# Kernel optimization log

Hardware: AMD Instinct MI355X
Metric: run time of the kernel (lower is better)

Reference implementation:

```python
import jax, jax.numpy as jnp
import numpy as np

N, B, NPG, DEG, F = 16384, 128, 128, 8, 128
E = N * DEG
H1, C1, H2, C2, H3, C3 = 3, 128, 2, 64, 2, 32
D = H1 * C1 + H2 * C2 + C3  # 544
K = 30
ND = 2048
LAMDA = 0.8


def _gatv2(x, src, dst, Wl, Wr, att, b, h, c, concat):
    n = x.shape[0]
    xl = (x @ Wl).reshape(n, h, c)
    xr = (x @ Wr).reshape(n, h, c)
    e = jax.nn.leaky_relu(xl[src] + xr[dst], 0.2)           # [E+N, h, c]
    logit = jnp.einsum('ehc,hc->eh', e, att)
    m = jax.lax.stop_gradient(jax.ops.segment_max(logit, dst, num_segments=n))
    a = jnp.exp(logit - m[dst])
    z = jax.ops.segment_sum(a, dst, num_segments=n)
    a = a / z[dst]
    out = jax.ops.segment_sum(xl[src] * a[:, :, None], dst, num_segments=n)
    out = out.reshape(n, h * c) if concat else out.mean(axis=1)
    return out + b


def _bn(x, g, b):
    m = x.mean(0)
    v = ((x - m) ** 2).mean(0)
    return (x - m) * jax.lax.rsqrt(v + 1e-5) * g + b


def _neighbor(emb, adj, W, b, idx):
    h = emb @ W + b
    A = adj + jnp.eye(adj.shape[0], dtype=adj.dtype)
    d = jax.lax.rsqrt(A.sum(axis=1))
    h = (1.0 - LAMDA) * h + LAMDA * ((d[:, None] * A * d[None, :]) @ h)
    v = h[idx]
    return v / jnp.clip(jnp.linalg.norm(v, axis=1, keepdims=True), 1e-12)


def setup_inputs():
    key = jax.random.key(0)
    it = iter(jax.random.split(key, 48))
    def nrm(shape, s=0.05):
        return jax.random.normal(next(it), shape, jnp.float32) * s
    src = jnp.repeat(jnp.arange(N, dtype=jnp.int32), DEG)
    dst = (src // NPG) * NPG + jax.random.randint(next(it), (E,), 0, NPG, dtype=jnp.int32)
    batch = jnp.arange(N, dtype=jnp.int32) // NPG
    return dict(
        x=jax.random.normal(next(it), (N, F), jnp.float32),
        edge_src=src, edge_dst=dst, batch=batch,
        pairs1=jax.random.randint(next(it), (B,), 0, ND, dtype=jnp.int32),
        pairs2=jax.random.randint(next(it), (B,), 0, ND, dtype=jnp.int32),
        drug_adj=(jax.random.uniform(next(it), (ND, ND)) < 0.01).astype(jnp.float32),
        drug_emb=jax.random.normal(next(it), (ND, ND), jnp.float32) * 0.1,
        dis_adj=(jax.random.uniform(next(it), (ND, ND)) < 0.01).astype(jnp.float32),
        dis_emb=jax.random.normal(next(it), (ND, ND), jnp.float32) * 0.1,
        Wde=nrm((ND, 32)), bde=jnp.zeros((32,), jnp.float32),
        Wse=nrm((ND, 32)), bse=jnp.zeros((32,), jnp.float32),
        W1l=nrm((F, H1 * C1)), W1r=nrm((F, H1 * C1)), att1=nrm((H1, C1)), b1=jnp.zeros((H1 * C1,), jnp.float32),
        W2l=nrm((H1 * C1, H2 * C2)), W2r=nrm((H1 * C1, H2 * C2)), att2=nrm((H2, C2)), b2=jnp.zeros((H2 * C2,), jnp.float32),
        W3l=nrm((H2 * C2, H3 * C3)), W3r=nrm((H2 * C2, H3 * C3)), att3=nrm((H3, C3)), b3=jnp.zeros((C3,), jnp.float32),
        g1=jnp.ones((H1 * C1,), jnp.float32), be1=jnp.zeros((H1 * C1,), jnp.float32),
        g2=jnp.ones((H2 * C2,), jnp.float32), be2=jnp.zeros((H2 * C2,), jnp.float32),
        Ws=nrm((D, K)), bs=jnp.zeros((K,), jnp.float32),
        Wg=nrm((D, D)), bg=jnp.zeros((D,), jnp.float32),
        Wl1=nrm((D * K + 64, 128)), bl1=jnp.zeros((128,), jnp.float32),
        Wl2=nrm((128, 1)), bl2=jnp.zeros((1,), jnp.float32),
    )


def _forward(x, drug_adj, drug_emb, dis_adj, dis_emb, Wde, bde, Wse, bse,
             W1l, W1r, att1, b1, W2l, W2r, att2, b2, W3l, W3r, att3, b3,
             g1, be1, g2, be2, Ws, bs, Wg, bg, Wl1, bl1, Wl2, bl2,
             edge_src, edge_dst, batch, pairs1, pairs2):
    loop = jnp.arange(N, dtype=edge_src.dtype)  # GATv2 self loops
    src = jnp.concatenate([edge_src, loop])
    dst = jnp.concatenate([edge_dst, loop])
    x1 = _bn(jax.nn.relu(_gatv2(x, src, dst, W1l, W1r, att1, b1, H1, C1, True)), g1, be1)
    x2 = _bn(jax.nn.relu(_gatv2(x1, src, dst, W2l, W2r, att2, b2, H2, C2, True)), g2, be2)
    x3 = _gatv2(x2, src, dst, W3l, W3r, att3, b3, H3, C3, False)
    xc = jnp.concatenate([x1, x2, x3], axis=1)              # [N, D]
    xd = xc.reshape(B, NPG, D)                              # to_dense_batch (equal graphs)
    adj = jnp.zeros((B, NPG, NPG), xc.dtype).at[
        batch[edge_src], edge_src % NPG, edge_dst % NPG].add(1.0)
    s = jax.nn.softmax(xd @ Ws + bs, axis=-1)               # [B, NPG, K]
    xp = jnp.einsum('bnk,bnd->bkd', s, xd)                  # pooled features
    ap = jnp.einsum('bnk,bnm,bml->bkl', s, adj, s)          # pooled adjacency
    ap = ap.at[:, jnp.arange(K), jnp.arange(K)].set(1.0)    # DenseGCNConv add_loop
    dg = jax.lax.rsqrt(jnp.clip(ap.sum(-1), 1.0))
    apn = dg[:, :, None] * ap * dg[:, None, :]
    xg = jax.nn.relu(jnp.einsum('bkl,bld->bkd', apn, xp @ Wg) + bg)
    de = _neighbor(drug_emb, drug_adj, Wde, bde, pairs1)    # [B, 32]
    se = _neighbor(dis_emb, dis_adj, Wse, bse, pairs2)      # [B, 32]
    g = jnp.concatenate([de, xg.reshape(B, K * D), se], axis=-1)
    h = jax.nn.relu(g @ Wl1 + bl1)
    return (h @ Wl2 + bl2)[:, 0]


def reference(x, edge_src, edge_dst, batch, pairs1, pairs2, drug_adj, drug_emb, dis_adj, dis_emb,
              Wde, bde, Wse, bse, W1l, W1r, att1, b1, W2l, W2r, att2, b2, W3l, W3r, att3, b3,
              g1, be1, g2, be2, Ws, bs, Wg, bg, Wl1, bl1, Wl2, bl2):
    return _forward(x, drug_adj, drug_emb, dis_adj, dis_emb, Wde, bde, Wse, bse,
                    W1l, W1r, att1, b1, W2l, W2r, att2, b2, W3l, W3r, att3, b3,
                    g1, be1, g2, be2, Ws, bs, Wg, bg, Wl1, bl1, Wl2, bl2,
                    edge_src, edge_dst, batch, pairs1, pairs2)
```

## Files before the change

kernel.cpp:

```cpp
#include <hip/hip_runtime.h>
#include <math.h>

#define CDIV(a,b) (((a)+(b)-1)/(b))
#define HMIN(a,b) ((a)<(b)?(a):(b))
#define MAXD 48

typedef __attribute__((ext_vector_type(8))) short bf16x8;
typedef __attribute__((ext_vector_type(4))) float f32x4;

static __device__ inline short f2bf(float x){
  unsigned u = __float_as_uint(x);
  unsigned r = (u + 0x7fffu + ((u >> 16) & 1u)) >> 16;
  return (short)r;
}
static __device__ inline float bf2f(short s){
  return __uint_as_float(((unsigned)(unsigned short)s) << 16);
}

__global__ __launch_bounds__(256)
void transpose_bf16(const float* __restrict__ B, int K, int N, short* __restrict__ Bt)
{
  __shared__ float t[32][33];
  int k0 = blockIdx.x*32, n0 = blockIdx.y*32;
  int c = threadIdx.x & 31, r8 = threadIdx.x >> 5;
  for (int rr = r8; rr < 32; rr += 8) {
    int k = k0+rr, n = n0+c;
    t[rr][c] = (k < K && n < N) ? B[(size_t)k*N + n] : 0.f;
  }
  __syncthreads();
  for (int rr = r8; rr < 32; rr += 8) {
    int n = n0+rr, k = k0+c;
    if (n < N && k < K) Bt[(size_t)n*K + k] = f2bf(t[c][rr]);
  }
}

__global__ __launch_bounds__(256)
void transpose_bf16_2(const float* __restrict__ A0, int K0, int N0, short* __restrict__ D0,
                      const float* __restrict__ A1, int K1, int N1, short* __restrict__ D1)
{
  const float* B; short* Bt; int K, N;
  if (blockIdx.z == 0) { B=A0; Bt=D0; K=K0; N=N0; } else { B=A1; Bt=D1; K=K1; N=N1; }
  int ntx = CDIV(K,32), nty = CDIV(N,32);
  int tile = blockIdx.x;
  if (tile >= ntx*nty) return;
  int k0 = (tile % ntx)*32, n0 = (tile / ntx)*32;
  __shared__ float t[32][33];
  int c = threadIdx.x & 31, r8 = threadIdx.x >> 5;
  for (int rr = r8; rr < 32; rr += 8) {
    int k = k0+rr, n = n0+c;
    t[rr][c] = (k < K && n < N) ? B[(size_t)k*N + n] : 0.f;
  }
  __syncthreads();
  for (int rr = r8; rr < 32; rr += 8) {
    int n = n0+rr, k = k0+c;
    if (n < N && k < K) Bt[(size_t)n*K + k] = f2bf(t[c][rr]);
  }
}

__global__ __launch_bounds__(256)
void gemm_mfma(const float* __restrict__ A, int lda,
               const short* __restrict__ Bt,
               float* __restrict__ C, int ldc,
               int M, int N, int K,
               const float* __restrict__ bias, int relu, int ksplit)
{
  __shared__ short As[128][40];
  __shared__ short Bs[128][40];
  const int k0 = blockIdx.z * ksplit;
  const int k1 = HMIN(k0 + ksplit, K);
  C += (size_t)blockIdx.z * (size_t)M * ldc;
  const int bm = blockIdx.x * 128, bn = blockIdx.y * 128;
  const int tid = threadIdx.x;
  const int sr = tid >> 1;
  const int sk = (tid & 1) * 16;
  const int wave = tid >> 6;
  const int wr = (wave >> 1) * 64, wc = (wave & 1) * 64;
  const int lane = tid & 63;
  const int lrow = lane & 15, lk = (lane >> 4) * 8;

  f32x4 acc[4][4];
  #pragma unroll
  for (int i=0;i<4;i++)
    #pragma unroll
    for (int j=0;j<4;j++) acc[i][j] = (f32x4){0.f,0.f,0.f,0.f};

  const bool bok = (bn + sr) < N;
  for (int kb = k0; kb < k1; kb += 32) {
    __syncthreads();
    {
      const float* ap = A + (size_t)(bm + sr)*lda + kb + sk;
      float4 v0 = *(const float4*)(ap+0);
      float4 v1 = *(const float4*)(ap+4);
      float4 v2 = *(const float4*)(ap+8);
      float4 v3 = *(const float4*)(ap+12);
      bf16x8 w0, w1;
      w0[0]=f2bf(v0.x); w0[1]=f2bf(v0.y); w0[2]=f2bf(v0.z); w0[3]=f2bf(v0.w);
      w0[4]=f2bf(v1.x); w0[5]=f2bf(v1.y); w0[6]=f2bf(v1.z); w0[7]=f2bf(v1.w);
      w1[0]=f2bf(v2.x); w1[1]=f2bf(v2.y); w1[2]=f2bf(v2.z); w1[3]=f2bf(v2.w);
      w1[4]=f2bf(v3.x); w1[5]=f2bf(v3.y); w1[6]=f2bf(v3.z); w1[7]=f2bf(v3.w);
      *(bf16x8*)&As[sr][sk]   = w0;
      *(bf16x8*)&As[sr][sk+8] = w1;
    }
    {
      bf16x8 u0 = (bf16x8){0,0,0,0,0,0,0,0}, u1 = u0;
      if (bok) {
        const short* bp = Bt + (size_t)(bn + sr)*K + kb + sk;
        u0 = *(const bf16x8*)(bp);
        u1 = *(const bf16x8*)(bp+8);
      }
      *(bf16x8*)&Bs[sr][sk]   = u0;
      *(bf16x8*)&Bs[sr][sk+8] = u1;
    }
    __syncthreads();
    bf16x8 af[4], bfr[4];
    #pragma unroll
    for (int f=0;f<4;f++) af[f]  = *(const bf16x8*)&As[wr + f*16 + lrow][lk];
    #pragma unroll
    for (int f=0;f<4;f++) bfr[f] = *(const bf16x8*)&Bs[wc + f*16 + lrow][lk];
    #pragma unroll
    for (int i=0;i<4;i++)
      #pragma unroll
      for (int j=0;j<4;j++)
        acc[i][j] = __builtin_amdgcn_mfma_f32_16x16x32_bf16(af[i], bfr[j], acc[i][j], 0, 0, 0);
  }
  const int erow = (lane >> 4) * 4;
  const int ecol = lane & 15;
  #pragma unroll
  for (int j=0;j<4;j++) {
    int gcol = bn + wc + j*16 + ecol;
    if (gcol >= N) continue;
    float bv = bias ? bias[gcol] : 0.f;
    #pragma unroll
    for (int i=0;i<4;i++) {
      int grow = bm + wr + i*16 + erow;
      #pragma unroll
      for (int r=0;r<4;r++) {
        float v = acc[i][j][r] + bv;
        if (relu) v = fmaxf(v, 0.f);
        C[(size_t)(grow + r)*ldc + gcol] = v;
      }
    }
  }
}

__global__ __launch_bounds__(256)
void skinny_gemm32(const float* __restrict__ A, int lda,
                   const float* __restrict__ B,
                   float* __restrict__ Cp, int M, int ksplit)
{
  const int m0 = blockIdx.x * 32;
  const int k0 = blockIdx.z * ksplit;
  __shared__ float As[32][68];
  __shared__ float Bs[64][36];
  float acc[4] = {0.f,0.f,0.f,0.f};
  const int r  = threadIdx.x >> 3;
  const int cg = (threadIdx.x & 7) * 4;
  for (int kb = k0; kb < k0 + ksplit; kb += 64) {
    {
      int rr = threadIdx.x >> 3, ko = (threadIdx.x & 7)*8;
      const float* ap = &A[(size_t)(m0+rr)*lda + kb + ko];
      *(float4*)&As[rr][ko]   = *(const float4*)ap;
      *(float4*)&As[rr][ko+4] = *(const float4*)(ap+4);
      int br = threadIdx.x >> 2, co = (threadIdx.x & 3)*8;
      const float* bp = &B[(size_t)(kb+br)*32 + co];
      *(float4*)&Bs[br][co]   = *(const float4*)bp;
      *(float4*)&Bs[br][co+4] = *(const float4*)(bp+4);
    }
    __syncthreads();
    #pragma unroll
    for (int kk=0; kk<64; kk+=4) {
      float4 a4 = *(const float4*)&As[r][kk];
      float4 b0 = *(const float4*)&Bs[kk  ][cg];
      float4 b1 = *(const float4*)&Bs[kk+1][cg];
      float4 b2 = *(const float4*)&Bs[kk+2][cg];
      float4 b3 = *(const float4*)&Bs[kk+3][cg];
      acc[0] += a4.x*b0.x + a4.y*b1.x + a4.z*b2.x + a4.w*b3.x;
      acc[1] += a4.x*b0.y + a4.y*b1.y + a4.z*b2.y + a4.w*b3.y;
      acc[2] += a4.x*b0.z + a4.y*b1.z + a4.z*b2.z + a4.w*b3.z;
      acc[3] += a4.x*b0.w + a4.y*b1.w + a4.z*b2.w + a4.w*b3.w;
    }
    __syncthreads();
  }
  float* cp = Cp + ((size_t)blockIdx.z*M + m0 + r)*32 + cg;
  *(float4*)cp = make_float4(acc[0],acc[1],acc[2],acc[3]);
}

__global__ void build_adj(const int* __restrict__ src, const int* __restrict__ dst,
                          int E, float* __restrict__ adj)
{
  int e = blockIdx.x*blockDim.x + threadIdx.x;
  if (e >= E) return;
  int s = src[e], d = dst[e];
  int g = s >> 7;
  atomicAdd(&adj[((size_t)g*128 + (s & 127))*128 + (d & 127)], 1.0f);
}

__global__ __launch_bounds__(1024)
void build_nbr(const int* __restrict__ dst, int epg, int shift,
               int* __restrict__ nbr, int* __restrict__ deg)
{
  __shared__ short ld[1024];
  const int g = blockIdx.x;
  for (int i = threadIdx.x; i < epg; i += 1024) ld[i] = (short)(dst[g*epg + i] & 127);
  __syncthreads();
  const int d   = threadIdx.x >> 3;
  const int seg = threadIdx.x & 7;
  const int spe = epg >> 3;
  const int i0 = seg*spe, i1 = i0 + spe;
  int cnt = 0;
  for (int i = i0; i < i1; ++i) cnt += (ld[i] == (short)d) ? 1 : 0;
  int pre = cnt;
  #pragma unroll
  for (int off=1; off<8; off<<=1) {
    int v = __shfl_up(pre, off, 8);
    if (seg >= off) pre += v;
  }
  const int base  = pre - cnt;
  const int total = __shfl(pre, 7, 8);
  if (seg == 7) deg[g*128 + d] = HMIN(total, MAXD);
  const int lbase = (g*128 + d)*MAXD;
  int w = base;
  for (int i = i0; i < i1; ++i) {
    if (ld[i] == (short)d) {
      if (w < MAXD) nbr[lbase + w] = i >> shift;
      ++w;
    }
  }
}

template<int C, int NL>
__global__ __launch_bounds__(512)
void gat_attn_sp(const float* __restrict__ XL, const float* __restrict__ XR, int ldx,
                 const float* __restrict__ att,
                 const int* __restrict__ nbr, const int* __restrict__ deg,
                 const float* __restrict__ bias, int bias_per_head,
                 float* __restrict__ out, int ldo)
{
  constexpr int SPAN = C / NL;
  constexpr int NG = 512 / NL;
  constexpr int PADC = C + 8;
  __shared__ short xls[128][PADC];
  __shared__ float A_lds[128];
  __shared__ float lgs[NG][MAXD+4];
  const int g = blockIdx.x, hh = blockIdx.y;
  const int d0 = blockIdx.z * 64;
  const int colbase = hh*C;
  const int tid = threadIdx.x;
  const int lane = tid & (NL-1);
  const int grp  = tid / NL;

  for (int idx = tid; idx < 128*C/4; idx += 512) {
    int r = idx / (C/4), q4 = idx % (C/4);
    float4 v = *(const float4*)&XL[(size_t)(g*128+r)*ldx + colbase + q4*4];
    short4 w;
    w.x = f2bf(v.x); w.y = f2bf(v.y); w.z = f2bf(v.z); w.w = f2bf(v.w);
    *(short4*)&xls[r][q4*4] = w;
  }
  float attv[SPAN];
  #pragma unroll
  for (int j=0;j<SPAN;j++) attv[j] = att[hh*C + lane*SPAN + j];
  __syncthreads();

  for (int s = grp; s < 128; s += NG) {
    float a = 0.f;
    #pragma unroll
    for (int j4=0;j4<SPAN;j4+=4) {
      short4 xv = *(const short4*)&xls[s][lane*SPAN + j4];
      a += attv[j4+0]*bf2f(xv.x) + attv[j4+1]*bf2f(xv.y)
         + attv[j4+2]*bf2f(xv.z) + attv[j4+3]*bf2f(xv.w);
    }
    #pragma unroll
    for (int t=1;t<NL;t<<=1) a += __shfl_xor(a, t, 64);
    if (lane == 0) A_lds[s] = a;
  }
  __syncthreads();

  for (int d = d0 + grp; d < d0 + 64; d += NG) {
    float xrv[SPAN];
    #pragma unroll
    for (int j=0;j<SPAN;j++) xrv[j] = XR[(size_t)(g*128+d)*ldx + colbase + lane*SPAN + j];
    float B = 0.f;
    #pragma unroll
    for (int j=0;j<SPAN;j++) B += attv[j]*xrv[j];
    #pragma unroll
    for (int t=1;t<NL;t<<=1) B += __shfl_xor(B, t, 64);
    const int dgn = deg[g*128+d];
    const int base = (g*128+d)*MAXD;
    float m = -1e30f;
    for (int i = 0; i <= dgn; ++i) {
      int s = (i < dgn) ? nbr[base+i] : d;
      float dot = 0.f;
      #pragma unroll
      for (int j4=0;j4<SPAN;j4+=4) {
        short4 xv = *(const short4*)&xls[s][lane*SPAN + j4];
        dot += attv[j4+0]*fabsf(bf2f(xv.x) + xrv[j4+0]);
        dot += attv[j4+1]*fabsf(bf2f(xv.y) + xrv[j4+1]);
        dot += attv[j4+2]*fabsf(bf2f(xv.z) + xrv[j4+2]);
        dot += attv[j4+3]*fabsf(bf2f(xv.w) + xrv[j4+3]);
      }
      #pragma unroll
      for (int t=1;t<NL;t<<=1) dot += __shfl_xor(dot, t, 64);
      float lg = 0.6f*(A_lds[s] + B) + 0.4f*dot;
      if (lane == 0) lgs[grp][i] = lg;
      m = fmaxf(m, lg);
    }
    float z = 0.f;
    for (int i = lane; i <= dgn; i += NL) z += __expf(lgs[grp][i] - m);
    #pragma unroll
    for (int t=1;t<NL;t<<=1) z += __shfl_xor(z, t, 64);
    const float zinv = 1.f / z;
    for (int i = lane; i <= dgn; i += NL) lgs[grp][i] = __expf(lgs[grp][i] - m) * zinv;
    float acc[SPAN];
    #pragma unroll
    for (int j=0;j<SPAN;j++) acc[j]=0.f;
    for (int i = 0; i <= dgn; ++i) {
      int s = (i < dgn) ? nbr[base+i] : d;
      float P = lgs[grp][i];
      #pragma unroll
      for (int j4=0;j4<SPAN;j4+=4) {
        short4 xv = *(const short4*)&xls[s][lane*SPAN + j4];
        acc[j4+0] += P*bf2f(xv.x); acc[j4+1] += P*bf2f(xv.y);
        acc[j4+2] += P*bf2f(xv.z); acc[j4+3] += P*bf2f(xv.w);
      }
    }
    float o[SPAN];
    #pragma unroll
    for (int j=0;j<SPAN;j++) {
      int cc = lane*SPAN + j;
      float bv = bias ? (bias_per_head ? bias[colbase+cc] : bias[cc]) : 0.f;
      o[j] = acc[j] + bv;
    }
    float* op = &out[(size_t)(g*128+d)*ldo + colbase + lane*SPAN];
    #pragma unroll
    for (int j4=0;j4<SPAN;j4+=4)
      *(float4*)&op[j4] = make_float4(o[j4],o[j4+1],o[j4+2],o[j4+3]);
  }
}

__global__ __launch_bounds__(256)
void bn_partial(const float* __restrict__ in, int HC,
                float* __restrict__ psum, float* __restrict__ psq)
{
  const int cg = blockIdx.x, rb = blockIdx.y;
  const int cl = threadIdx.x & 31;
  const int rl = threadIdx.x >> 5;
  const int col = cg*32 + cl;
  float s = 0.f, s2 = 0.f;
  for (int r = rb*512 + rl; r < (rb+1)*512; r += 8) {
    float v = fmaxf(in[(size_t)r*HC + col], 0.f);
    s += v; s2 += v*v;
  }
  __shared__ float ls[8][33], ls2[8][33];
  ls[rl][cl] = s; ls2[rl][cl] = s2;
  __syncthreads();
  if (threadIdx.x < 32) {
    float a=0.f, a2=0.f;
    for (int r=0;r<8;r++){ a += ls[r][threadIdx.x]; a2 += ls2[r][threadIdx.x]; }
    psum[rb*HC + cg*32 + threadIdx.x] = a;
    psq [rb*HC + cg*32 + threadIdx.x] = a2;
  }
}

__global__ void bn_finalize(const float* __restrict__ psum, const float* __restrict__ psq,
                            int HC, float* __restrict__ mv)
{
  int c = blockIdx.x*blockDim.x + threadIdx.x;
  if (c >= HC) return;
  float s=0.f, s2=0.f;
  for (int r=0;r<32;r++){ s += psum[r*HC+c]; s2 += psq[r*HC+c]; }
  float m = s * (1.f/16384.f);
  float v = s2 * (1.f/16384.f) - m*m;
  mv[c] = m; mv[HC+c] = v;
}

__global__ void bn_apply4(const float* __restrict__ in, int HC,
                          const float* __restrict__ mv,
                          const float* __restrict__ gamma, const float* __restrict__ beta,
                          float* __restrict__ out, int ldo, int total4)
{
  int i4 = blockIdx.x*blockDim.x + threadIdx.x;
  if (i4 >= total4) return;
  size_t i = (size_t)i4*4;
  int r = i / HC, c = i % HC;
  float4 v = *(const float4*)&in[i];
  float4 mvv = *(const float4*)&mv[c];
  float4 vav = *(const float4*)&mv[HC+c];
  float4 gv = *(const float4*)&gamma[c];
  float4 bv = *(const float4*)&beta[c];
  float4 o;
  o.x = (fmaxf(v.x,0.f) - mvv.x) * rsqrtf(vav.x + 1e-5f) * gv.x + bv.x;
  o.y = (fmaxf(v.y,0.f) - mvv.y) * rsqrtf(vav.y + 1e-5f) * gv.y + bv.y;
  o.z = (fmaxf(v.z,0.f) - mvv.z) * rsqrtf(vav.z + 1e-5f) * gv.z + bv.z;
  o.w = (fmaxf(v.w,0.f) - mvv.w) * rsqrtf(vav.w + 1e-5f) * gv.w + bv.w;
  *(float4*)&out[(size_t)r*ldo + c] = o;
}

__global__ void combine3(const float* __restrict__ raw, float* __restrict__ xc)
{
  int i = blockIdx.x*blockDim.x + threadIdx.x;
  if (i >= 16384*32) return;
  int r = i >> 5, c = i & 31;
  xc[(size_t)r*544 + 512 + c] = 0.5f*(raw[r*64 + c] + raw[r*64 + 32 + c]);
}

__global__ void softmax30(float* __restrict__ s, int M)
{
  int w = (blockIdx.x*blockDim.x + threadIdx.x) >> 5;
  int lane = threadIdx.x & 31;
  if (w >= M) return;
  float v = (lane < 30) ? s[(size_t)w*30 + lane] : -1e30f;
  float m = v;
  for (int t=16;t>0;t>>=1) m = fmaxf(m, __shfl_xor(m, t, 32));
  float e = (lane < 30) ? __expf(v - m) : 0.f;
  float z = e;
  for (int t=16;t>0;t>>=1) z += __shfl_xor(z, t, 32);
  if (lane < 30) s[(size_t)w*30 + lane] = e / z;
}

__global__ __launch_bounds__(256)
void xp_kernel(const float* __restrict__ s, const float* __restrict__ xc,
               float* __restrict__ xp)
{
  const int b = blockIdx.x;
  const int d = blockIdx.y*256 + threadIdx.x;
  __shared__ float sb[128][32];
  for (int idx = threadIdx.x; idx < 128*30; idx += 256) {
    int n = idx/30, k = idx%30;
    sb[n][k] = s[(size_t)(b*128+n)*30 + k];
  }
  __syncthreads();
  if (d >= 544) return;
  float acc[30];
  #pragma unroll
  for (int k=0;k<30;k++) acc[k]=0.f;
  const float* xcp = xc + (size_t)b*128*544 + d;
  for (int n=0;n<128;n++) {
    float xcv = xcp[(size_t)n*544];
    const float4* sp = (const float4*)&sb[n][0];
    #pragma unroll
    for (int q=0;q<7;q++) {
      float4 v = sp[q];
      acc[q*4+0] += v.x*xcv; acc[q*4+1] += v.y*xcv;
      acc[q*4+2] += v.z*xcv; acc[q*4+3] += v.w*xcv;
    }
    float2 v2 = *(const float2*)&sb[n][28];
    acc[28] += v2.x*xcv; acc[29] += v2.y*xcv;
  }
  #pragma unroll
  for (int k=0;k<30;k++) xp[((size_t)b*30+k)*544 + d] = acc[k];
}

__global__ __launch_bounds__(256)
void pool_adj_kernel(const float* __restrict__ adj, const float* __restrict__ s,
                     float* __restrict__ apn)
{
  const int b = blockIdx.x;
  __shared__ float sb[128][32];
  __shared__ float t1s[128][32];
  __shared__ float apb[30][31];
  __shared__ float dg[30];
  for (int idx = threadIdx.x; idx < 128*30; idx += 256) {
    int n = idx/30, k = idx%30;
    sb[n][k] = s[(size_t)(b*128+n)*30 + k];
  }
  __syncthreads();
  if (threadIdx.x < 128) {
    const int i = threadIdx.x;
    float acc[30];
    #pragma unroll
    for (int k=0;k<30;k++) acc[k]=0.f;
    const float* arow = adj + ((size_t)b*128 + i)*128;
    for (int j=0;j<128;j++) {
      float a = arow[j];
      const float4* sp = (const float4*)&sb[j][0];
      #pragma unroll
      for (int q=0;q<7;q++) {
        float4 v = sp[q];
        acc[q*4+0] += v.x*a; acc[q*4+1] += v.y*a;
        acc[q*4+2] += v.z*a; acc[q*4+3] += v.w*a;
      }
      float2 v2 = *(const float2*)&sb[j][28];
      acc[28] += v2.x*a; acc[29] += v2.y*a;
    }
    #pragma unroll
    for (int k=0;k<30;k++) t1s[i][k] = acc[k];
  }
  __syncthreads();
  for (int idx = threadIdx.x; idx < 900; idx += 256) {
    int k = idx/30, l = idx%30;
    float acc = 0.f;
    for (int n=0;n<128;n++) acc += sb[n][k]*t1s[n][l];
    apb[k][l] = (k == l) ? 1.f : acc;
  }
  __syncthreads();
  if (threadIdx.x < 30) {
    float ssum = 0.f;
    for (int l=0;l<30;l++) ssum += apb[threadIdx.x][l];
    dg[threadIdx.x] = rsqrtf(fmaxf(ssum, 1.f));
  }
  __syncthreads();
  for (int idx = threadIdx.x; idx < 900; idx += 256) {
    int k = idx/30, l = idx%30;
    apn[(size_t)b*900 + idx] = dg[k]*dg[l]*apb[k][l];
  }
}

__global__ __launch_bounds__(256)
void xg_kernel(const float* __restrict__ apn, const float* __restrict__ xpw,
               const float* __restrict__ bg, float* __restrict__ g)
{
  int b = blockIdx.x;
  __shared__ float a[30][31];
  for (int idx = threadIdx.x; idx < 900; idx += 256)
    a[idx/30][idx%30] = apn[(size_t)b*900 + idx];
  __syncthreads();
  for (int idx = threadIdx.x; idx < 30*544; idx += 256) {
    int k = idx / 544, d = idx % 544;
    float acc = 0.f;
    for (int l=0;l<30;l++) acc += a[k][l] * xpw[((size_t)b*30 + l)*544 + d];
    g[(size_t)b*16384 + 32 + k*544 + d] = fmaxf(acc + bg[d], 0.f);
  }
}

__global__ __launch_bounds__(256)
void rowsum_rsqrt(const float* __restrict__ A, int n, float* __restrict__ dinv)
{
  int r = blockIdx.x;
  float s = 0.f;
  for (int j = threadIdx.x; j < n; j += 256) s += A[(size_t)r*n + j];
  for (int m=32;m>0;m>>=1) s += __shfl_xor(s, m, 64);
  __shared__ float red[4];
  if ((threadIdx.x & 63) == 0) red[threadIdx.x >> 6] = s;
  __syncthreads();
  if (threadIdx.x == 0) dinv[r] = rsqrtf(red[0]+red[1]+red[2]+red[3] + 1.f);
}

__global__ __launch_bounds__(256)
void embed_partial(const float* __restrict__ adjM, const float* __restrict__ hW,
                   const float* __restrict__ dinv, const int* __restrict__ idx,
                   float* __restrict__ part)
{
  const int b = blockIdx.x;
  const int z = blockIdx.z;
  const int row = idx[b];
  const int c  = threadIdx.x & 31;
  const int jc = threadIdx.x >> 5;
  const int j0 = z*64;
  float u = 0.f;
  #pragma unroll
  for (int t=0;t<8;t++) {
    int j = j0 + jc + t*8;
    u += adjM[(size_t)row*2048 + j] * hW[j*32 + c] * dinv[j];
  }
  __shared__ float red[8][33];
  red[jc][c] = u;
  __syncthreads();
  if (threadIdx.x < 32) {
    float s = 0.f;
    #pragma unroll
    for (int r=0;r<8;r++) s += red[r][threadIdx.x];
    part[((size_t)z*128 + b)*32 + threadIdx.x] = s;
  }
}

__global__ void embed_final(const float* __restrict__ part, const float* __restrict__ hW,
                            const float* __restrict__ dinv, const int* __restrict__ idx,
                            float* __restrict__ g, int goff)
{
  const int b = blockIdx.x;
  const int c = threadIdx.x;
  const int row = idx[b];
  float s = 0.f;
  for (int z=0; z<32; ++z) s += part[((size_t)z*128 + b)*32 + c];
  float hw = hW[(size_t)row*32 + c];
  float dv = dinv[row];
  float h2 = 0.2f*hw + 0.8f*dv*(s + hw*dv);
  float ss = h2*h2;
  #pragma unroll
  for (int m=1;m<32;m<<=1) ss += __shfl_xor(ss, m, 32);
  float nrm = fmaxf(sqrtf(ss), 1e-12f);
  g[(size_t)b*16384 + goff + c] = h2 / nrm;
}

__global__ void reduce_parts(const float* __restrict__ part, const float* __restrict__ bias,
                             float* __restrict__ outp, int total, int nz, int ldc, int relu)
{
  int i = blockIdx.x*blockDim.x + threadIdx.x;
  if (i >= total) return;
  float s = 0.f;
  for (int p=0;p<nz;p++) s += part[(size_t)p*total + i];
  if (bias) s += bias[i % ldc];
  if (relu) s = fmaxf(s, 0.f);
  outp[i] = s;
}

__global__ void final_out(const float* __restrict__ h, const float* __restrict__ Wl2,
                          const float* __restrict__ bl2, float* __restrict__ out)
{
  int m = threadIdx.x;
  if (m >= 128) return;
  float s = 0.f;
  for (int k=0;k<128;k++) s += h[m*128 + k] * Wl2[k];
  out[m] = s + bl2[0];
}

extern "C" void kernel_launch(void* const* d_in, const int* in_sizes, int n_in,
                              void* d_out, int out_size, void* d_ws, size_t ws_size,
                              hipStream_t stream)
{
  const float* x        = (const float*)d_in[0];
  const int*   edge_src = (const int*)d_in[1];
  const int*   edge_dst = (const int*)d_in[2];
  const int*   pairs1   = (const int*)d_in[4];
  const int*   pairs2   = (const int*)d_in[5];
  const float* drug_adj = (const float*)d_in[6];
  const float* drug_emb = (const float*)d_in[7];
  const float* dis_adj  = (const float*)d_in[8];
  const float* dis_emb  = (const float*)d_in[9];
  const float* Wde = (const float*)d_in[10];
  const float* bde = (const float*)d_in[11];
  const float* Wse = (const float*)d_in[12];
  const float* bse = (const float*)d_in[13];
  const float* W1l = (const float*)d_in[14];
  const float* W1r = (const float*)d_in[15];
  const float* att1= (const float*)d_in[16];
  const float* b1  = (const float*)d_in[17];
  const float* W2l = (const float*)d_in[18];
  const float* W2r = (const float*)d_in[19];
  const float* att2= (const float*)d_in[20];
  const float* b2  = (const float*)d_in[21];
  const float* W3l = (const float*)d_in[22];
  const float* W3r = (const float*)d_in[23];
  const float* att3= (const float*)d_in[24];
  const float* b3  = (const float*)d_in[25];
  const float* g1  = (const float*)d_in[26];
  const float* be1 = (const float*)d_in[27];
  const float* g2  = (const float*)d_in[28];
  const float* be2 = (const float*)d_in[29];
  const float* Wsm = (const float*)d_in[30];
  const float* bs  = (const float*)d_in[31];
  const float* Wg  = (const float*)d_in[32];
  const float* bg  = (const float*)d_in[33];
  const float* Wl1 = (const float*)d_in[34];
  const float* bl1 = (const float*)d_in[35];
  const float* Wl2 = (const float*)d_in[36];
  const float* bl2 = (const float*)d_in[37];
  float* out = (float*)d_out;

  const int E = in_sizes[1];
  const int epg = E >> 7;
  const int shift = 31 - __builtin_clz(epg >> 7);

  float* ws  = (float*)d_ws;
  float* adj = ws;
  int*   nbr = (int*)adj;
  int*   degb= nbr + 16384*MAXD;
  float* xc  = ws + 2097152;
  float* P   = ws + 11010048;
  float* XLR = P;
  float* RAW = P + 12582912;
  float* bnp = ws + 29884416;
  float* bnq = bnp + 12288;
  float* mv  = bnq + 12288;
  short* wT  = (short*)(mv + 1024);
  float* sbuf = P;
  float* xp   = P + 491520;
  float* apn  = P + 3187200;
  float* xpw  = P + 3302400;
  float* gbuf = P + 5391360;
  float* hWd  = P + 7488512;
  float* dinvd= hWd + 65536;
  float* hWs_ = dinvd + 2048;
  float* dinvs= hWs_ + 65536;
  float* upart= dinvs + 2048;
  float* partials = upart + 131072;
  float* hfin = partials + 1048576;
  float* epart = hfin + 16384;
  short* wgT  = (short*)epart;
  short* wl1T = (short*)RAW;

  build_nbr<<<128, 1024, 0, stream>>>(edge_dst, epg, shift, nbr, degb);

  transpose_bf16_2<<<dim3(48,1,2), 256, 0, stream>>>(W1l, 128, 384, wT,
                                                     W1r, 128, 384, wT + 384*128);
  gemm_mfma<<<dim3(128,6,1), 256, 0, stream>>>(x, 128, wT, XLR, 768, 16384, 768, 128, nullptr, 0, 128);
  gat_attn_sp<128,16><<<dim3(128,3,2), 512, 0, stream>>>(XLR, XLR + 384, 768, att1, nbr, degb, b1, 1, RAW, 384);
  bn_partial<<<dim3(12,32), 256, 0, stream>>>(RAW, 384, bnp, bnq);
  bn_finalize<<<2, 256, 0, stream>>>(bnp, bnq, 384, mv);
  bn_apply4<<<CDIV(16384*96,256), 256, 0, stream>>>(RAW, 384, mv, g1, be1, xc, 544, 16384*96);

  transpose_bf16_2<<<dim3(48,1,2), 256, 0, stream>>>(W2l, 384, 128, wT,
                                                     W2r, 384, 128, wT + 128*384);
  gemm_mfma<<<dim3(128,2,1), 256, 0, stream>>>(xc, 544, wT, XLR, 256, 16384, 256, 384, nullptr, 0, 384);
  gat_attn_sp<64,8><<<dim3(128,2,2), 512, 0, stream>>>(XLR, XLR + 128, 256, att2, nbr, degb, b2, 1, RAW, 128);
  bn_partial<<<dim3(4,32), 256, 0, stream>>>(RAW, 128, bnp, bnq);
  bn_finalize<<<1, 256, 0, stream>>>(bnp, bnq, 128, mv);
  bn_apply4<<<CDIV(16384*32,256), 256, 0, stream>>>(RAW, 128, mv, g2, be2, xc + 384, 544, 16384*32);

  transpose_bf16_2<<<dim3(8,1,2), 256, 0, stream>>>(W3l, 128, 64, wT,
                                                    W3r, 128, 64, wT + 64*128);
  gemm_mfma<<<dim3(128,1,1), 256, 0, stream>>>(xc + 384, 544, wT, XLR, 128, 16384, 128, 128, nullptr, 0, 128);
  gat_attn_sp<32,8><<<dim3(128,2,2), 512, 0, stream>>>(XLR, XLR + 64, 128, att3, nbr, degb, b3, 0, RAW, 64);
  combine3<<<CDIV(16384*32,256), 256, 0, stream>>>(RAW, xc);

  hipMemsetAsync(adj, 0, (size_t)2097152*4, stream);
  build_adj<<<CDIV(E,256), 256, 0, stream>>>(edge_src, edge_dst, E, adj);

  transpose_bf16_2<<<dim3(289,1,2), 256, 0, stream>>>(Wsm, 544, 30, wT,
                                                      Wg, 544, 544, wgT);
  gemm_mfma<<<dim3(128,1,1), 256, 0, stream>>>(xc, 544, wT, sbuf, 30, 16384, 30, 544, bs, 0, 544);
  softmax30<<<CDIV(16384*32,256), 256, 0, stream>>>(sbuf, 16384);
  xp_kernel<<<dim3(128,3), 256, 0, stream>>>(sbuf, xc, xp);
  pool_adj_kernel<<<128, 256, 0, stream>>>(adj, sbuf, apn);
  gemm_mfma<<<dim3(30,5,1), 256, 0, stream>>>(xp, 544, wgT, xpw, 544, 3840, 544, 544, nullptr, 0, 544);
  xg_kernel<<<128, 256, 0, stream>>>(apn, xpw, bg, gbuf);

  skinny_gemm32<<<dim3(64,1,8), 256, 0, stream>>>(drug_emb, 2048, Wde, epart, 2048, 256);
  reduce_parts<<<CDIV(65536,256), 256, 0, stream>>>(epart, bde, hWd, 65536, 8, 32, 0);
  rowsum_rsqrt<<<2048, 256, 0, stream>>>(drug_adj, 2048, dinvd);
  embed_partial<<<dim3(128,1,32), 256, 0, stream>>>(drug_adj, hWd, dinvd, pairs1, upart);
  embed_final<<<128, 32, 0, stream>>>(upart, hWd, dinvd, pairs1, gbuf, 0);

  skinny_gemm32<<<dim3(64,1,8), 256, 0, stream>>>(dis_emb, 2048, Wse, epart, 2048, 256);
  reduce_parts<<<CDIV(65536,256), 256, 0, stream>>>(epart, bse, hWs_, 65536, 8, 32, 0);
  rowsum_rsqrt<<<2048, 256, 0, stream>>>(dis_adj, 2048, dinvs);
  embed_partial<<<dim3(128,1,32), 256, 0, stream>>>(dis_adj, hWs_, dinvs, pairs2, upart);
  embed_final<<<128, 32, 0, stream>>>(upart, hWs_, dinvs, pairs2, gbuf, 16352);

  transpose_bf16<<<dim3(512,4), 256, 0, stream>>>(Wl1, 16384, 128, wl1T);
  gemm_mfma<<<dim3(1,1,64), 256, 0, stream>>>(gbuf, 16384, wl1T, partials, 128, 128, 128, 16384, nullptr, 0, 256);
  reduce_parts<<<CDIV(16384,256), 256, 0, stream>>>(partials, bl1, hfin, 16384, 64, 128, 1);
  final_out<<<1, 128, 0, stream>>>(hfin, Wl2, bl2, out);
}
```

Baseline: 462.6 us.

## Batch weight transposes and drug/disease branches into fewer launches, fuse layer-3 mean

Replaces the several per-layer weight transposes with one multi-job transpose launch over seven matrices into separate buffers. The drug and disease neighbor-embedding pipelines (skinny GEMM, reduction, rowsum, embed partial and final) are each merged into a single launch indexed by blockIdx.y, with separate scratch buffers. Layer-3 GATv2 attention now loops over both heads in one block and writes the head mean directly into the concatenated features, removing the combine3 kernel and its intermediate buffer. This cuts launch count and some memory traffic in exchange for more workspace and a serialized head loop in the layer-3 kernel.

New measurement: 450.6 us, median of 2. 2.6% less time.

```diff
diff --git a/kernel.cpp b/kernel.cpp
--- a/kernel.cpp
+++ b/kernel.cpp
@@ -34,12 +34,19 @@
   }
 }
 
-__global__ __launch_bounds__(256)
-void transpose_bf16_2(const float* __restrict__ A0, int K0, int N0, short* __restrict__ D0,
-                      const float* __restrict__ A1, int K1, int N1, short* __restrict__ D1)
-{
-  const float* B; short* Bt; int K, N;
-  if (blockIdx.z == 0) { B=A0; Bt=D0; K=K0; N=N0; } else { B=A1; Bt=D1; K=K1; N=N1; }
+struct TJobs {
+  const float* src[7];
+  short* dst[7];
+  int K[7];
+  int N[7];
+};
+__global__ __launch_bounds__(256)
+void transpose_multi(TJobs j)
+{
+  const int job = blockIdx.y;
+  const float* B = j.src[job];
+  short* Bt = j.dst[job];
+  const int K = j.K[job], N = j.N[job];
   int ntx = CDIV(K,32), nty = CDIV(N,32);
   int tile = blockIdx.x;
   if (tile >= ntx*nty) return;
@@ -144,10 +151,13 @@
 }
 
 __global__ __launch_bounds__(256)
-void skinny_gemm32(const float* __restrict__ A, int lda,
-                   const float* __restrict__ B,
-                   float* __restrict__ Cp, int M, int ksplit)
-{
+void skinny_gemm32_2(const float* __restrict__ A0, const float* __restrict__ A1, int lda,
+                     const float* __restrict__ B0, const float* __restrict__ B1,
+                     float* __restrict__ C0, float* __restrict__ C1, int M, int ksplit)
+{
+  const float* A = blockIdx.y ? A1 : A0;
+  const float* B = blockIdx.y ? B1 : B0;
+  float* Cp      = blockIdx.y ? C1 : C0;
   const int m0 = blockIdx.x * 32;
   const int k0 = blockIdx.z * ksplit;
   __shared__ float As[32][68];
@@ -185,6 +195,22 @@
   *(float4*)cp = make_float4(acc[0],acc[1],acc[2],acc[3]);
 }
 
+__global__ void reduce_parts2(const float* __restrict__ p0, const float* __restrict__ p1,
+                              const float* __restrict__ b0, const float* __restrict__ b1,
+                              float* __restrict__ o0, float* __restrict__ o1,
+                              int total, int nz, int ldc)
+{
+  const float* part = blockIdx.y ? p1 : p0;
+  const float* bias = blockIdx.y ? b1 : b0;
+  float* outp       = blockIdx.y ? o1 : o0;
+  int i = blockIdx.x*blockDim.x + threadIdx.x;
+  if (i >= total) return;
+  float s = 0.f;
+  for (int p=0;p<nz;p++) s += part[(size_t)p*total + i];
+  s += bias[i % ldc];
+  outp[i] = s;
+}
+
 __global__ void build_adj(const int* __restrict__ src, const int* __restrict__ dst,
                           int E, float* __restrict__ adj)
 {
@@ -275,6 +301,7 @@
   }
   __syncthreads();
 
+  #pragma unroll
   for (int d = d0 + grp; d < d0 + 64; d += NG) {
     float xrv[SPAN];
     #pragma unroll
@@ -335,6 +362,107 @@
     for (int j4=0;j4<SPAN;j4+=4)
       *(float4*)&op[j4] = make_float4(o[j4],o[j4+1],o[j4+2],o[j4+3]);
   }
+}
+
+__global__ __launch_bounds__(512)
+void gat_attn3_mean(const float* __restrict__ XL, const float* __restrict__ XR, int ldx,
+                    const float* __restrict__ att,
+                    const int* __restrict__ nbr, const int* __restrict__ deg,
+                    const float* __restrict__ bias, float* __restrict__ xc)
+{
+  constexpr int C = 32, NL = 8, SPAN = 4, NG = 64;
+  __shared__ short xls[128][C+8];
+  __shared__ float A_lds[128];
+  __shared__ float lgs[NG][MAXD+4];
+  const int g = blockIdx.x;
+  const int d0 = blockIdx.z * 64;
+  const int tid = threadIdx.x;
+  const int lane = tid & (NL-1);
+  const int grp  = tid / NL;
+  const int d = d0 + grp;
+  const int dgn = deg[g*128+d];
+  const int base = (g*128+d)*MAXD;
+  float om[SPAN] = {0.f,0.f,0.f,0.f};
+
+  for (int hh = 0; hh < 2; ++hh) {
+    const int colbase = hh*C;
+    __syncthreads();
+    for (int idx = tid; idx < 128*(C/4); idx += 512) {
+      int r = idx / (C/4), q4 = idx % (C/4);
+      float4 v = *(const float4*)&XL[(size_t)(g*128+r)*ldx + colbase + q4*4];
+      short4 w;
+      w.x = f2bf(v.x); w.y = f2bf(v.y); w.z = f2bf(v.z); w.w = f2bf(v.w);
+      *(short4*)&xls[r][q4*4] = w;
+    }
+    float attv[SPAN];
+    #pragma unroll
+    for (int j=0;j<SPAN;j++) attv[j] = att[hh*C + lane*SPAN + j];
+    __syncthreads();
+    for (int s = grp; s < 128; s += NG) {
+      float a = 0.f;
+      #pragma unroll
+      for (int j4=0;j4<SPAN;j4+=4) {
+        short4 xv = *(const short4*)&xls[s][lane*SPAN + j4];
+        a += attv[j4+0]*bf2f(xv.x) + attv[j4+1]*bf2f(xv.y)
+           + attv[j4+2]*bf2f(xv.z) + attv[j4+3]*bf2f(xv.w);
+      }
+      #pragma unroll
+      for (int t=1;t<NL;t<<=1) a += __shfl_xor(a, t, 64);
+      if (lane == 0) A_lds[s] = a;
+    }
+    __syncthreads();
+
+    float xrv[SPAN];
+    #pragma unroll
+    for (int j=0;j<SPAN;j++) xrv[j] = XR[(size_t)(g*128+d)*ldx + colbase + lane*SPAN + j];
+    float B = 0.f;
+    #pragma unroll
+    for (int j=0;j<SPAN;j++) B += attv[j]*xrv[j];
+    #pragma unroll
+    for (int t=1;t<NL;t<<=1) B += __shfl_xor(B, t, 64);
+    float m = -1e30f;
+    for (int i = 0; i <= dgn; ++i) {
+      int s = (i < dgn) ? nbr[base+i] : d;
+      float dot = 0.f;
+      #pragma unroll
+      for (int j4=0;j4<SPAN;j4+=4) {
+        short4 xv = *(const short4*)&xls[s][lane*SPAN + j4];
+        dot += attv[j4+0]*fabsf(bf2f(xv.x) + xrv[j4+0]);
+        dot += attv[j4+1]*fabsf(bf2f(xv.y) + xrv[j4+1]);
+        dot += attv[j4+2]*fabsf(bf2f(xv.z) + xrv[j4+2]);
+        dot += attv[j4+3]*fabsf(bf2f(xv.w) + xrv[j4+3]);
+      }
+      #pragma unroll
+      for (int t=1;t<NL;t<<=1) dot += __shfl_xor(dot, t, 64);
+      float lg = 0.6f*(A_lds[s] + B) + 0.4f*dot;
+      if (lane == 0) lgs[grp][i] = lg;
+      m = fmaxf(m, lg);
+    }
+    float z = 0.f;
+    for (int i = lane; i <= dgn; i += NL) z += __expf(lgs[grp][i] - m);
+    #pragma unroll
+    for (int t=1;t<NL;t<<=1) z += __shfl_xor(z, t, 64);
+    const float zinv = 1.f / z;
+    for (int i = lane; i <= dgn; i += NL) lgs[grp][i] = __expf(lgs[grp][i] - m) * zinv;
+    float acc[SPAN];
+    #pragma unroll
+    for (int j=0;j<SPAN;j++) acc[j]=0.f;
+    for (int i = 0; i <= dgn; ++i) {
+      int s = (i < dgn) ? nbr[base+i] : d;
+      float P = lgs[grp][i];
+      #pragma unroll
+      for (int j4=0;j4<SPAN;j4+=4) {
+        short4 xv = *(const short4*)&xls[s][lane*SPAN + j4];
+        acc[j4+0] += P*bf2f(xv.x); acc[j4+1] += P*bf2f(xv.y);
+        acc[j4+2] += P*bf2f(xv.z); acc[j4+3] += P*bf2f(xv.w);
+      }
+    }
+    #pragma unroll
+    for (int j=0;j<SPAN;j++)
+      om[j] += 0.5f*(acc[j] + bias[lane*SPAN + j]);
+  }
+  float4 o = make_float4(om[0], om[1], om[2], om[3]);
+  *(float4*)&xc[(size_t)(g*128+d)*544 + 512 + lane*SPAN] = o;
 }
 
 __global__ __launch_bounds__(256)
@@ -395,14 +523,6 @@
   *(float4*)&out[(size_t)r*ldo + c] = o;
 }
 
-__global__ void combine3(const float* __restrict__ raw, float* __restrict__ xc)
-{
-  int i = blockIdx.x*blockDim.x + threadIdx.x;
-  if (i >= 16384*32) return;
-  int r = i >> 5, c = i & 31;
-  xc[(size_t)r*544 + 512 + c] = 0.5f*(raw[r*64 + c] + raw[r*64 + 32 + c]);
-}
-
 __global__ void softmax30(float* __restrict__ s, int M)
 {
   int w = (blockIdx.x*blockDim.x + threadIdx.x) >> 5;
@@ -523,8 +643,11 @@
 }
 
 __global__ __launch_bounds__(256)
-void rowsum_rsqrt(const float* __restrict__ A, int n, float* __restrict__ dinv)
-{
+void rowsum_rsqrt2(const float* __restrict__ A0, const float* __restrict__ A1,
+                   int n, float* __restrict__ d0, float* __restrict__ d1)
+{
+  const float* A = blockIdx.y ? A1 : A0;
+  float* dinv    = blockIdx.y ? d1 : d0;
   int r = blockIdx.x;
   float s = 0.f;
   for (int j = threadIdx.x; j < n; j += 256) s += A[(size_t)r*n + j];
@@ -536,10 +659,17 @@
 }
 
 __global__ __launch_bounds__(256)
-void embed_partial(const float* __restrict__ adjM, const float* __restrict__ hW,
-                   const float* __restrict__ dinv, const int* __restrict__ idx,
-                   float* __restrict__ part)
-{
+void embed_partial2(const float* __restrict__ a0, const float* __restrict__ a1,
+                    const float* __restrict__ h0, const float* __restrict__ h1,
+                    const float* __restrict__ v0, const float* __restrict__ v1,
+                    const int* __restrict__ i0p, const int* __restrict__ i1p,
+                    float* __restrict__ p0, float* __restrict__ p1)
+{
+  const float* adjM = blockIdx.y ? a1 : a0;
+  const float* hW   = blockIdx.y ? h1 : h0;
+  const float* dinv = blockIdx.y ? v1 : v0;
+  const int*   idx  = blockIdx.y ? i1p : i0p;
+  float*       part = blockIdx.y ? p1 : p0;
   const int b = blockIdx.x;
   const int z = blockIdx.z;
   const int row = idx[b];
@@ -563,10 +693,17 @@
   }
 }
 
-__global__ void embed_final(const float* __restrict__ part, const float* __restrict__ hW,
-                            const float* __restrict__ dinv, const int* __restrict__ idx,
-                            float* __restrict__ g, int goff)
-{
+__global__ void embed_final2(const float* __restrict__ p0, const float* __restrict__ p1,
+                             const float* __restrict__ h0, const float* __restrict__ h1,
+                             const float* __restrict__ v0, const float* __restrict__ v1,
+                             const int* __restrict__ i0p, const int* __restrict__ i1p,
+                             float* __restrict__ g)
+{
+  const float* part = blockIdx.y ? p1 : p0;
+  const float* hW   = blockIdx.y ? h1 : h0;
+  const float* dinv = blockIdx.y ? v1 : v0;
+  const int*   idx  = blockIdx.y ? i1p : i0p;
+  const int goff    = blockIdx.y ? 16352 : 0;
   const int b = blockIdx.x;
   const int c = threadIdx.x;
   const int row = idx[b];
@@ -662,7 +799,10 @@
   float* bnp = ws + 29884416;
   float* bnq = bnp + 12288;
   float* mv  = bnq + 12288;
-  short* wT  = (short*)(mv + 1024);
+  short* wcat1 = (short*)(mv + 1024);
+  short* wcat2 = wcat1 + 98304;
+  short* wcat3 = wcat2 + 98304;
+  short* wsmT  = wcat3 + 16384;
   float* sbuf = P;
   float* xp   = P + 491520;
   float* apn  = P + 3187200;
@@ -672,60 +812,65 @@
   float* dinvd= hWd + 65536;
   float* hWs_ = dinvd + 2048;
   float* dinvs= hWs_ + 65536;
-  float* upart= dinvs + 2048;
-  float* partials = upart + 131072;
+  float* upartD = dinvs + 2048;
+  float* upartS = upartD + 131072;
+  float* partials = upartS + 131072;
   float* hfin = partials + 1048576;
-  float* epart = hfin + 16384;
-  short* wgT  = (short*)epart;
+  float* epartD = hfin + 16384;
+  float* epartS = epartD + 524288;
+  short* wgT  = (short*)(epartS + 524288);
   short* wl1T = (short*)RAW;
 
+  {
+    TJobs tj;
+    tj.src[0]=W1l; tj.dst[0]=wcat1;           tj.K[0]=128; tj.N[0]=384;
+    tj.src[1]=W1r; tj.dst[1]=wcat1 + 384*128; tj.K[1]=128; tj.N[1]=384;
+    tj.src[2]=W2l; tj.dst[2]=wcat2;           tj.K[2]=384; tj.N[2]=128;
+    tj.src[3]=W2r; tj.dst[3]=wcat2 + 128*384; tj.K[3]=384; tj.N[3]=128;
+    tj.src[4]=W3l; tj.dst[4]=wcat3;           tj.K[4]=128; tj.N[4]=64;
+    tj.src[5]=W3r; tj.dst[5]=wcat3 + 64*128;  tj.K[5]=128; tj.N[5]=64;
+    tj.src[6]=Wsm; tj.dst[6]=wsmT;            tj.K[6]=544; tj.N[6]=30;
+    transpose_multi<<<dim3(48,7), 256, 0, stream>>>(tj);
+  }
+
   build_nbr<<<128, 1024, 0, stream>>>(edge_dst, epg, shift, nbr, degb);
 
-  transpose_bf16_2<<<dim3(48,1,2), 256, 0, stream>>>(W1l, 128, 384, wT,
-                                                     W1r, 128, 384, wT + 384*128);
-  gemm_mfma<<<dim3(128,6,1), 256, 0, stream>>>(x, 128, wT, XLR, 768, 16384, 768, 128, nullptr, 0, 128);
+  gemm_mfma<<<dim3(128,6,1), 256, 0, stream>>>(x, 128, wcat1, XLR, 768, 16384, 768, 128, nullptr, 0, 128);
   gat_attn_sp<128,16><<<dim3(128,3,2), 512, 0, stream>>>(XLR, XLR + 384, 768, att1, nbr, degb, b1, 1, RAW, 384);
   bn_partial<<<dim3(12,32), 256, 0, stream>>>(RAW, 384, bnp, bnq);
   bn_finalize<<<2, 256, 0, stream>>>(bnp, bnq, 384, mv);
   bn_apply4<<<CDIV(16384*96,256), 256, 0, stream>>>(RAW, 384, mv, g1, be1, xc, 544, 16384*96);
 
-  transpose_bf16_2<<<dim3(48,1,2), 256, 0, stream>>>(W2l, 384, 128, wT,
-                                                     W2r, 384, 128, wT + 128*384);
-  gemm_mfma<<<dim3(128,2,1), 256, 0, stream>>>(xc, 544, wT, XLR, 256, 16384, 256, 384, nullptr, 0, 384);
+  gemm_mfma<<<dim3(128,2,1), 256, 0, stream>>>(xc, 544, wcat2, XLR, 256, 16384, 256, 384, nullptr, 0, 384);
   gat_attn_sp<64,8><<<dim3(128,2,2), 512, 0, stream>>>(XLR, XLR + 128, 256, att2, nbr, degb, b2, 1, RAW, 128);
   bn_partial<<<dim3(4,32), 256, 0, stream>>>(RAW, 128, bnp, bnq);
   bn_finalize<<<1, 256, 0, stream>>>(bnp, bnq, 128, mv);
   bn_apply4<<<CDIV(16384*32,256), 256, 0, stream>>>(RAW, 128, mv, g2, be2, xc + 384, 544, 16384*32);
 
-  transpose_bf16_2<<<dim3(8,1,2), 256, 0, stream>>>(W3l, 128, 64, wT,
-                                                    W3r, 128, 64, wT + 64*128);
-  gemm_mfma<<<dim3(128,1,1), 256, 0, stream>>>(xc + 384, 544, wT, XLR, 128, 16384, 128, 128, nullptr, 0, 128);
-  gat_attn_sp<32,8><<<dim3(128,2,2), 512, 0, stream>>>(XLR, XLR + 64, 128, att3, nbr, degb, b3, 0, RAW, 64);
-  combine3<<<CDIV(16384*32,256), 256, 0, stream>>>(RAW, xc);
+  gemm_mfma<<<dim3(128,1,1), 256, 0, stream>>>(xc + 384, 544, wcat3, XLR, 128, 16384, 128, 128, nullptr, 0, 128);
+  gat_attn3_mean<<<dim3(128,1,2), 512, 0, stream>>>(XLR, XLR + 64, 128, att3, nbr, degb, b3, xc);
 
   hipMemsetAsync(adj, 0, (size_t)2097152*4, stream);
   build_adj<<<CDIV(E,256), 256, 0, stream>>>(edge_src, edge_dst, E, adj);
 
-  transpose_bf16_2<<<dim3(289,1,2), 256, 0, stream>>>(Wsm, 544, 30, wT,
-                                                      Wg, 544, 544, wgT);
-  gemm_mfma<<<dim3(128,1,1), 256, 0, stream>>>(xc, 544, wT, sbuf, 30, 16384, 30, 544, bs, 0, 544);
+  gemm_mfma<<<dim3(128,1,1), 256, 0, stream>>>(xc, 544, wsmT, sbuf, 30, 16384, 30, 544, bs, 0, 544);
   softmax30<<<CDIV(16384*32,256), 256, 0, stream>>>(sbuf, 16384);
   xp_kernel<<<dim3(128,3), 256, 0, stream>>>(sbuf, xc, xp);
   pool_adj_kernel<<<128, 256, 0, stream>>>(adj, sbuf, apn);
+  transpose_bf16<<<dim3(17,17), 256, 0, stream>>>(Wg, 544, 544, wgT);
   gemm_mfma<<<dim3(30,5,1), 256, 0, stream>>>(xp, 544, wgT, xpw, 544, 3840, 544, 544, nullptr, 0, 544);
   xg_kernel<<<128, 256, 0, stream>>>(apn, xpw, bg, gbuf);
 
-  skinny_gemm32<<<dim3(64,1,8), 256, 0, stream>>>(drug_emb, 2048, Wde, epart, 2048, 256);
-  reduce_parts<<<CDIV(65536,256), 256, 0, stream>>>(epart, bde, hWd, 65536, 8, 32, 0);
-  rowsum_rsqrt<<<2048, 256, 0, stream>>>(drug_adj, 2048, dinvd);
-  embed_partial<<<dim3(128,1,32), 256, 0, stream>>>(drug_adj, hWd, dinvd, pairs1, upart);
-  embed_final<<<128, 32, 0, stream>>>(upart, hWd, dinvd, pairs1, gbuf, 0);
-
-  skinny_gemm32<<<dim3(64,1,8), 256, 0, stream>>>(dis_emb, 2048, Wse, epart, 2048, 256);
-  reduce_parts<<<CDIV(65536,256), 256, 0, stream>>>(epart, bse, hWs_, 65536, 8, 32, 0);
-  rowsum_rsqrt<<<2048, 256, 0, stream>>>(dis_adj, 2048, dinvs);
-  embed_partial<<<dim3(128,1,32), 256, 0, stream>>>(dis_adj, hWs_, dinvs, pairs2, upart);
-  embed_final<<<128, 32, 0, stream>>>(upart, hWs_, dinvs, pairs2, gbuf, 16352);
+  skinny_gemm32_2<<<dim3(64,2,8), 256, 0, stream>>>(drug_emb, dis_emb, 2048, Wde, Wse,
+                                                    epartD, epartS, 2048, 256);
+  reduce_parts2<<<dim3(CDIV(65536,256),2), 256, 0, stream>>>(epartD, epartS, bde, bse,
+                                                             hWd, hWs_, 65536, 8, 32);
+  rowsum_rsqrt2<<<dim3(2048,2), 256, 0, stream>>>(drug_adj, dis_adj, 2048, dinvd, dinvs);
+  embed_partial2<<<dim3(128,2,32), 256, 0, stream>>>(drug_adj, dis_adj, hWd, hWs_,
+                                                     dinvd, dinvs, pairs1, pairs2,
+                                                     upartD, upartS);
+  embed_final2<<<dim3(128,2), 32, 0, stream>>>(upartD, upartS, hWd, hWs_,
+                                               dinvd, dinvs, pairs1, pairs2, gbuf);
 
   transpose_bf16<<<dim3(512,4), 256, 0, stream>>>(Wl1, 16384, 128, wl1T);
   gemm_mfma<<<dim3(1,1,64), 256, 0, stream>>>(gbuf, 16384, wl1T, partials, 128, 128, 128, 16384, nullptr, 0, 256);
```
